# Performance work log

Hardware: AMD Instinct MI355X
Metric: run time of the kernel (lower is better)

The kernel has to match this reference:

```python
import jax, jax.numpy as jnp
import numpy as np

B, N, D_IN, D_OUT, R = 8, 1024, 256, 256, 4


def setup_inputs() -> dict:
    key = jax.random.key(0)
    ks = jax.random.split(key, 8)
    scale_in = 1.0 / np.sqrt(D_IN)
    scale_out = 1.0 / np.sqrt(2 * D_OUT)
    scale_g = 1.0 / np.sqrt(D_OUT)
    return {
        "node_features": jax.random.normal(ks[0], (B, N, D_IN), dtype=jnp.float32),
        "adj_matrix": jax.random.randint(ks[1], (B, R, N, N), 0, 2, dtype=jnp.int32),
        "rel_w": jax.random.uniform(ks[2], (R, D_OUT, D_IN), jnp.float32, -scale_in, scale_in),
        "rel_b": jax.random.uniform(ks[3], (R, D_OUT), jnp.float32, -scale_in, scale_in),
        "attn_w": jax.random.uniform(ks[4], (2 * D_OUT,), jnp.float32, -scale_out, scale_out),
        "attn_b": jax.random.uniform(ks[5], (), jnp.float32, -scale_out, scale_out),
        "gate_w": jax.random.uniform(ks[6], (D_OUT,), jnp.float32, -scale_g, scale_g),
        "gate_b": jax.random.uniform(ks[7], (), jnp.float32, -scale_g, scale_g),
    }


def reference(node_features, adj_matrix, rel_w, rel_b, attn_w, attn_b, gate_w, gate_b):
    # Per-relation projections: [B, R, N, D]
    feats = jnp.einsum('bni,rdi->brnd', node_features, rel_w) + rel_b[None, :, None, :]
    # attn_proj(cat([h_i, h_j])) == h_i @ w_i + h_j @ w_j + b  (linear over concat)
    d = feats.shape[-1]
    si = jnp.einsum('brnd,d->brn', feats, attn_w[:d])   # contribution of row node i
    sj = jnp.einsum('brnd,d->brn', feats, attn_w[d:])   # contribution of col node j
    score = si[:, :, :, None] + sj[:, :, None, :] + attn_b  # [B, R, N, N]
    score = jnp.where(adj_matrix == 0, jnp.float32(-1e9), score)
    attn = jax.nn.softmax(score, axis=-1)
    # Aggregate over relations: sum_r attn_r @ feats_r -> [B, N, D]
    agg = jnp.einsum('brnm,brmd->bnd', attn, feats)
    gate = jax.nn.sigmoid(jnp.einsum('bnd,d->bn', agg, gate_w) + gate_b)
    return gate[:, :, None] * agg
```

## Files before the change

### kernel.cpp

```cpp
#include <hip/hip_runtime.h>
#include <hip/hip_bf16.h>

#define B_ 8
#define N_ 1024
#define DIN 256
#define DOUT 256
#define R_ 4

typedef __attribute__((ext_vector_type(8))) short bf16x8;
typedef __attribute__((ext_vector_type(4))) float f32x4;
typedef __attribute__((ext_vector_type(4))) int i32x4;

__device__ __forceinline__ unsigned short f2bf(float f) {
    union { float f; unsigned int u; } v; v.f = f;
    unsigned int u = v.u;
    u += 0x7fffu + ((u >> 16) & 1u);
    return (unsigned short)(u >> 16);
}
__device__ __forceinline__ float bf2f(unsigned short h) {
    union { float f; unsigned int u; } v; v.u = ((unsigned int)h) << 16;
    return v.f;
}

__device__ __forceinline__ void gl_lds16(const void* g, void* l) {
    __builtin_amdgcn_global_load_lds(
        (const __attribute__((address_space(1))) unsigned int*)g,
        (__attribute__((address_space(3))) unsigned int*)l, 16, 0, 0);
}

__global__ __launch_bounds__(256) void k0_swz(const float* __restrict__ rw,
                                              unsigned short* __restrict__ swzW) {
    int t = blockIdx.x * 256 + threadIdx.x;
    int lane = t & 63, nb = (t >> 6) & 15, ks = (t >> 10) & 7, r = t >> 13;
    int m = lane & 15, q = lane >> 4;
    const float* src = rw + ((r * DOUT + nb * 16 + m) * DIN) + ks * 32 + q * 8;
    float4 v0 = *(const float4*)src;
    float4 v1 = *(const float4*)(src + 4);
    bf16x8 o;
    o[0] = (short)f2bf(v0.x); o[1] = (short)f2bf(v0.y);
    o[2] = (short)f2bf(v0.z); o[3] = (short)f2bf(v0.w);
    o[4] = (short)f2bf(v1.x); o[5] = (short)f2bf(v1.y);
    o[6] = (short)f2bf(v1.z); o[7] = (short)f2bf(v1.w);
    *(bf16x8*)(swzW + (long)t * 8) = o;
}

__global__ __launch_bounds__(256) void k1_proj(const float* __restrict__ node,
        const unsigned short* __restrict__ swzW, const float* __restrict__ rel_b,
        const float* __restrict__ attn_w,
        unsigned short* __restrict__ fswz, unsigned short* __restrict__ ebf) {
    __shared__ unsigned short Wbuf[2][8192];
    int bid = blockIdx.x;
    int nt = bid & 15, r = (bid >> 4) & 3, b = bid >> 6;
    int w = threadIdx.x >> 6, lane = threadIdx.x & 63;
    int m = lane & 15, q = lane >> 4;
    int n0 = nt * 64 + w * 16;

    const float* Abase = node + ((b * N_ + n0 + m) * DIN) + q * 8;
    const unsigned short* Wsrc = swzW + r * 65536;

#pragma unroll
    for (int i = 0; i < 4; i++)
        gl_lds16(Wsrc + (w * 4 + i) * 512 + lane * 8, &Wbuf[0][(w * 4 + i) * 512]);

    f32x4 acc[16];
#pragma unroll
    for (int i = 0; i < 16; i++) acc[i] = (f32x4)0.0f;

    float4 a0 = *(const float4*)(Abase);
    float4 a1 = *(const float4*)(Abase + 4);

    for (int ks = 0; ks < 8; ks++) {
        int cur = ks & 1;
        __syncthreads();
        if (ks < 7) {
#pragma unroll
            for (int i = 0; i < 4; i++)
                gl_lds16(Wsrc + ((ks + 1) * 16 + w * 4 + i) * 512 + lane * 8,
                         &Wbuf[cur ^ 1][(w * 4 + i) * 512]);
        }
        bf16x8 af;
        af[0] = (short)f2bf(a0.x); af[1] = (short)f2bf(a0.y);
        af[2] = (short)f2bf(a0.z); af[3] = (short)f2bf(a0.w);
        af[4] = (short)f2bf(a1.x); af[5] = (short)f2bf(a1.y);
        af[6] = (short)f2bf(a1.z); af[7] = (short)f2bf(a1.w);
        if (ks < 7) {
            a0 = *(const float4*)(Abase + (ks + 1) * 32);
            a1 = *(const float4*)(Abase + (ks + 1) * 32 + 4);
        }
#pragma unroll
        for (int nb = 0; nb < 16; nb++) {
            bf16x8 wf = *(const bf16x8*)(&Wbuf[cur][nb * 512 + lane * 8]);
            acc[nb] = __builtin_amdgcn_mfma_f32_16x16x32_bf16(af, wf, acc[nb], 0, 0, 0);
        }
    }

    float sj0 = 0.f, sj1 = 0.f, sj2 = 0.f, sj3 = 0.f;
    float bias[16], aw[16];
#pragma unroll
    for (int nb = 0; nb < 16; nb++) {
        int d = nb * 16 + m;
        bias[nb] = rel_b[r * DOUT + d];
        aw[nb] = attn_w[DOUT + d];
        sj0 += (acc[nb][0] + bias[nb]) * aw[nb];
        sj1 += (acc[nb][1] + bias[nb]) * aw[nb];
        sj2 += (acc[nb][2] + bias[nb]) * aw[nb];
        sj3 += (acc[nb][3] + bias[nb]) * aw[nb];
    }
#pragma unroll
    for (int mk = 1; mk <= 8; mk <<= 1) {
        sj0 += __shfl_xor(sj0, mk, 64);
        sj1 += __shfl_xor(sj1, mk, 64);
        sj2 += __shfl_xor(sj2, mk, 64);
        sj3 += __shfl_xor(sj3, mk, 64);
    }
    float e0 = __expf(sj0), e1 = __expf(sj1), e2 = __expf(sj2), e3 = __expf(sj3);

    int slice = b * R_ + r;
    int js = n0 >> 5;
    int jhi = (n0 >> 4) & 1;
    int qp = jhi * 2 + (q >> 1);
    int jj0 = (q & 1) * 4;
    unsigned short* fb = fswz + ((long)(slice * 32 + js) * 16) * 512
                       + qp * 128 + m * 8 + jj0;
#pragma unroll
    for (int nb = 0; nb < 16; nb++) {
        ushort4 o;
        o.x = f2bf((acc[nb][0] + bias[nb]) * e0);
        o.y = f2bf((acc[nb][1] + bias[nb]) * e1);
        o.z = f2bf((acc[nb][2] + bias[nb]) * e2);
        o.w = f2bf((acc[nb][3] + bias[nb]) * e3);
        *(ushort4*)(fb + nb * 512) = o;
    }
    if (m == 0) {
        ushort4 o;
        o.x = f2bf(e0); o.y = f2bf(e1); o.z = f2bf(e2); o.w = f2bf(e3);
        *(ushort4*)(ebf + slice * N_ + n0 + q * 4) = o;
    }
}

__global__ __launch_bounds__(256, 4) void k3_attn(const int* __restrict__ adj,
        const unsigned short* __restrict__ fswz, const unsigned short* __restrict__ ebf,
        unsigned short* __restrict__ aggU, float* __restrict__ lbuf) {
    __shared__ unsigned short Gbuf[2][8192];
    __shared__ unsigned short Ebuf[512];

    int bid = blockIdx.x;
    int slice = (bid & 7) * 4 + ((bid >> 3) & 3);
    int rest = bid >> 5;
    int it = rest & 15, jh = rest >> 4;
    int t = threadIdx.x, lane = t & 63, w = t >> 6;
    int m = lane & 15, q = lane >> 4;
    int i0b = it * 64;

    const unsigned short* fsl = fswz + ((size_t)(slice * 32 + jh * 16)) * 8192;
    const int* adjbase = adj + (size_t)slice * (N_ * N_)
                       + (size_t)(i0b + w * 16 + m) * N_ + jh * 512 + q * 8;
    const unsigned short* esl = ebf + slice * N_ + jh * 512;

#pragma unroll
    for (int i = 0; i < 4; i++)
        gl_lds16(fsl + (w * 4 + i) * 512 + lane * 8, &Gbuf[0][(w * 4 + i) * 512]);
    if (w == 0)
        gl_lds16(esl + lane * 8, &Ebuf[0]);

    i32x4 A0c = *(const i32x4*)(adjbase);
    i32x4 A1c = *(const i32x4*)(adjbase + 4);

    f32x4 acc[16];
#pragma unroll
    for (int i = 0; i < 16; i++) acc[i] = (f32x4)0.0f;
    float l = 0.f;

    for (int s = 0; s < 16; s++) {
        int cur = s & 1;
        __syncthreads();
        i32x4 A0n, A1n;
        if (s < 15) {
#pragma unroll
            for (int i = 0; i < 4; i++)
                gl_lds16(fsl + (size_t)(s + 1) * 8192 + (w * 4 + i) * 512 + lane * 8,
                         &Gbuf[cur ^ 1][(w * 4 + i) * 512]);
            A0n = *(const i32x4*)(adjbase + (s + 1) * 32);
            A1n = *(const i32x4*)(adjbase + (s + 1) * 32 + 4);
        }
        bf16x8 ev = *(const bf16x8*)(&Ebuf[s * 32 + q * 8]);
        int av[8] = {A0c.x, A0c.y, A0c.z, A0c.w, A1c.x, A1c.y, A1c.z, A1c.w};
        const int* ei = (const int*)&ev;
        bf16x8 af;
        int* afi = (int*)&af;
#pragma unroll
        for (int p = 0; p < 4; p++) {
            unsigned int msk = (av[2 * p] ? 0xffffu : 0u)
                             | (av[2 * p + 1] ? 0xffff0000u : 0u);
            afi[p] = (int)(msk & 0x3F803F80u);
            int me = ei[p] & (int)msk;
            union { int i; float f; } lo, hi;
            lo.i = me << 16;
            hi.i = me & (int)0xffff0000u;
            l += lo.f + hi.f;
        }
        const unsigned short* Gb = &Gbuf[cur][lane * 8];
#pragma unroll
        for (int nb = 0; nb < 16; nb++) {
            bf16x8 bfq = *(const bf16x8*)(Gb + nb * 512);
            acc[nb] = __builtin_amdgcn_mfma_f32_16x16x32_bf16(af, bfq, acc[nb], 0, 0, 0);
        }
        A0c = A0n; A1c = A1n;
    }

    l += __shfl_xor(l, 16, 64);
    l += __shfl_xor(l, 32, 64);
    int half = slice * 2 + jh;
    if (lane < 16)
        lbuf[half * N_ + i0b + w * 16 + lane] = l;

    unsigned short* ob = aggU + ((size_t)half * N_ + i0b + w * 16 + q * 4) * DOUT + m;
#pragma unroll
    for (int nb = 0; nb < 16; nb++) {
#pragma unroll
        for (int reg = 0; reg < 4; reg++)
            ob[(size_t)reg * DOUT + nb * 16] = f2bf(acc[nb][reg]);
    }
}

__global__ __launch_bounds__(256) void k4_out(const unsigned short* __restrict__ aggU,
        const float* __restrict__ lbuf, const float* __restrict__ gate_w,
        const float* __restrict__ gate_b, float* __restrict__ out) {
    __shared__ float red[4];
    int bid = blockIdx.x;
    int n = bid & 1023, b = bid >> 10;
    int d = threadIdx.x;
    float s = 0.f;
#pragma unroll
    for (int r = 0; r < R_; r++) {
        int sl = b * R_ + r;
        float a0 = bf2f(aggU[((size_t)(sl * 2 + 0) * N_ + n) * DOUT + d]);
        float a1 = bf2f(aggU[((size_t)(sl * 2 + 1) * N_ + n) * DOUT + d]);
        float lt = lbuf[(sl * 2 + 0) * N_ + n] + lbuf[(sl * 2 + 1) * N_ + n];
        float inv = (lt > 0.f) ? 1.0f / lt : 0.f;
        s += (a0 + a1) * inv;
    }
    float v = s * gate_w[d];
#pragma unroll
    for (int off = 32; off; off >>= 1) v += __shfl_down(v, off, 64);
    int lane = d & 63, wave = d >> 6;
    if (lane == 0) red[wave] = v;
    __syncthreads();
    float tot = red[0] + red[1] + red[2] + red[3];
    float g = 1.f / (1.f + __expf(-(tot + gate_b[0])));
    out[((long)(b * N_ + n)) * DOUT + d] = g * s;
}

extern "C" void kernel_launch(void* const* d_in, const int* in_sizes, int n_in,
                              void* d_out, int out_size, void* d_ws, size_t ws_size,
                              hipStream_t stream) {
    const float* node   = (const float*)d_in[0];
    const int*   adj    = (const int*)d_in[1];
    const float* rel_w  = (const float*)d_in[2];
    const float* rel_b  = (const float*)d_in[3];
    const float* attn_w = (const float*)d_in[4];
    const float* gate_w = (const float*)d_in[6];
    const float* gate_b = (const float*)d_in[7];
    float* out = (float*)d_out;

    char* ws = (char*)d_ws;
    unsigned short* swzW = (unsigned short*)ws;
    unsigned short* fswz = (unsigned short*)(ws + 524288);
    unsigned short* ebf  = (unsigned short*)(ws + 17301504);
    unsigned short* aggU = (unsigned short*)(ws + 17367040);
    float*          lbuf = (float*)(ws + 50921472);

    k0_swz<<<128, 256, 0, stream>>>(rel_w, swzW);
    k1_proj<<<512, 256, 0, stream>>>(node, swzW, rel_b, attn_w, fswz, ebf);
    k3_attn<<<1024, 256, 0, stream>>>(adj, fswz, ebf, aggU, lbuf);
    k4_out<<<8192, 256, 0, stream>>>(aggU, lbuf, gate_w, gate_b, out);
}
```

Measured before the change: 253.6 us.

## Split attention K-loop across wave pairs and normalize in-kernel, dropping half-partials

The attention kernel no longer splits the column range across blocks. Each block now covers 32 rows over all 1024 columns, and the two wave pairs take alternate 32-column steps. The pairs reduce their partial accumulators and row sums through LDS, and softmax normalization happens before the bf16 store. This halves the aggregate intermediate buffer, removes the lbuf array, and simplifies the output kernel's reads. The cost is that each wave idles on alternate steps and the loop has twice as many block-wide barriers.

```diff
diff --git a/kernel.cpp b/kernel.cpp
--- a/kernel.cpp
+++ b/kernel.cpp
@@ -140,106 +140,124 @@
 
 __global__ __launch_bounds__(256, 4) void k3_attn(const int* __restrict__ adj,
         const unsigned short* __restrict__ fswz, const unsigned short* __restrict__ ebf,
-        unsigned short* __restrict__ aggU, float* __restrict__ lbuf) {
+        unsigned short* __restrict__ aggN) {
     __shared__ unsigned short Gbuf[2][8192];
-    __shared__ unsigned short Ebuf[512];
+    __shared__ unsigned short Ebuf[1024];
+    __shared__ float Lx[2][64];
 
     int bid = blockIdx.x;
     int slice = (bid & 7) * 4 + ((bid >> 3) & 3);
-    int rest = bid >> 5;
-    int it = rest & 15, jh = rest >> 4;
+    int it = bid >> 5;
     int t = threadIdx.x, lane = t & 63, w = t >> 6;
     int m = lane & 15, q = lane >> 4;
-    int i0b = it * 64;
-
-    const unsigned short* fsl = fswz + ((size_t)(slice * 32 + jh * 16)) * 8192;
+    int g = w & 1;
+    int ph = w >> 1;
+    int i0 = it * 32 + g * 16;
+
+    const unsigned short* fsl = fswz + (size_t)slice * (32 * 8192);
     const int* adjbase = adj + (size_t)slice * (N_ * N_)
-                       + (size_t)(i0b + w * 16 + m) * N_ + jh * 512 + q * 8;
-    const unsigned short* esl = ebf + slice * N_ + jh * 512;
+                       + (size_t)(i0 + m) * N_ + q * 8;
+    const unsigned short* esl = ebf + slice * N_;
 
 #pragma unroll
     for (int i = 0; i < 4; i++)
         gl_lds16(fsl + (w * 4 + i) * 512 + lane * 8, &Gbuf[0][(w * 4 + i) * 512]);
-    if (w == 0)
-        gl_lds16(esl + lane * 8, &Ebuf[0]);
-
-    i32x4 A0c = *(const i32x4*)(adjbase);
-    i32x4 A1c = *(const i32x4*)(adjbase + 4);
+    if (w < 2)
+        gl_lds16(esl + w * 512 + lane * 8, &Ebuf[w * 512]);
+
+    i32x4 A0c = *(const i32x4*)(adjbase + ph * 32);
+    i32x4 A1c = *(const i32x4*)(adjbase + ph * 32 + 4);
 
     f32x4 acc[16];
 #pragma unroll
     for (int i = 0; i < 16; i++) acc[i] = (f32x4)0.0f;
     float l = 0.f;
 
-    for (int s = 0; s < 16; s++) {
+    for (int s = 0; s < 32; s++) {
         int cur = s & 1;
         __syncthreads();
-        i32x4 A0n, A1n;
-        if (s < 15) {
+        if (s < 31) {
 #pragma unroll
             for (int i = 0; i < 4; i++)
                 gl_lds16(fsl + (size_t)(s + 1) * 8192 + (w * 4 + i) * 512 + lane * 8,
                          &Gbuf[cur ^ 1][(w * 4 + i) * 512]);
-            A0n = *(const i32x4*)(adjbase + (s + 1) * 32);
-            A1n = *(const i32x4*)(adjbase + (s + 1) * 32 + 4);
-        }
-        bf16x8 ev = *(const bf16x8*)(&Ebuf[s * 32 + q * 8]);
-        int av[8] = {A0c.x, A0c.y, A0c.z, A0c.w, A1c.x, A1c.y, A1c.z, A1c.w};
-        const int* ei = (const int*)&ev;
-        bf16x8 af;
-        int* afi = (int*)&af;
-#pragma unroll
-        for (int p = 0; p < 4; p++) {
-            unsigned int msk = (av[2 * p] ? 0xffffu : 0u)
-                             | (av[2 * p + 1] ? 0xffff0000u : 0u);
-            afi[p] = (int)(msk & 0x3F803F80u);
-            int me = ei[p] & (int)msk;
-            union { int i; float f; } lo, hi;
-            lo.i = me << 16;
-            hi.i = me & (int)0xffff0000u;
-            l += lo.f + hi.f;
-        }
-        const unsigned short* Gb = &Gbuf[cur][lane * 8];
+        }
+        if ((s & 1) == ph) {
+            i32x4 A0n, A1n;
+            if (s < 30) {
+                A0n = *(const i32x4*)(adjbase + (s + 2) * 32);
+                A1n = *(const i32x4*)(adjbase + (s + 2) * 32 + 4);
+            }
+            bf16x8 ev = *(const bf16x8*)(&Ebuf[s * 32 + q * 8]);
+            int av[8] = {A0c.x, A0c.y, A0c.z, A0c.w, A1c.x, A1c.y, A1c.z, A1c.w};
+            const int* ei = (const int*)&ev;
+            bf16x8 af;
+            int* afi = (int*)&af;
+#pragma unroll
+            for (int p = 0; p < 4; p++) {
+                unsigned int msk = (av[2 * p] ? 0xffffu : 0u)
+                                 | (av[2 * p + 1] ? 0xffff0000u : 0u);
+                afi[p] = (int)(msk & 0x3F803F80u);
+                int me = ei[p] & (int)msk;
+                union { int i; float f; } lo, hi;
+                lo.i = me << 16;
+                hi.i = me & (int)0xffff0000u;
+                l += lo.f + hi.f;
+            }
+            const unsigned short* Gb = &Gbuf[cur][lane * 8];
+#pragma unroll
+            for (int nb = 0; nb < 16; nb++) {
+                bf16x8 bfq = *(const bf16x8*)(Gb + nb * 512);
+                acc[nb] = __builtin_amdgcn_mfma_f32_16x16x32_bf16(af, bfq, acc[nb], 0, 0, 0);
+            }
+            if (s < 30) { A0c = A0n; A1c = A1n; }
+        }
+    }
+
+    __syncthreads();
+    if (w >= 2) {
+        float* GF = (float*)&Gbuf[0][0];
+#pragma unroll
+        for (int nb = 0; nb < 16; nb++)
+            *(f32x4*)(&GF[g * 4096 + nb * 256 + lane * 4]) = acc[nb];
+        Lx[g][lane] = l;
+    }
+    __syncthreads();
+    if (w < 2) {
+        const float* GF = (const float*)&Gbuf[0][0];
+#pragma unroll
+        for (int nb = 0; nb < 16; nb++)
+            acc[nb] += *(const f32x4*)(&GF[g * 4096 + nb * 256 + lane * 4]);
+        l += Lx[g][lane];
+        l += __shfl_xor(l, 16, 64);
+        l += __shfl_xor(l, 32, 64);
+        float linv[4];
+#pragma unroll
+        for (int reg = 0; reg < 4; reg++) {
+            float lr = __shfl(l, q * 4 + reg, 64);
+            linv[reg] = (lr > 0.f) ? 1.0f / lr : 0.f;
+        }
+        unsigned short* ob = aggN + ((size_t)(slice * N_ + i0 + q * 4)) * DOUT + m;
 #pragma unroll
         for (int nb = 0; nb < 16; nb++) {
-            bf16x8 bfq = *(const bf16x8*)(Gb + nb * 512);
-            acc[nb] = __builtin_amdgcn_mfma_f32_16x16x32_bf16(af, bfq, acc[nb], 0, 0, 0);
-        }
-        A0c = A0n; A1c = A1n;
-    }
-
-    l += __shfl_xor(l, 16, 64);
-    l += __shfl_xor(l, 32, 64);
-    int half = slice * 2 + jh;
-    if (lane < 16)
-        lbuf[half * N_ + i0b + w * 16 + lane] = l;
-
-    unsigned short* ob = aggU + ((size_t)half * N_ + i0b + w * 16 + q * 4) * DOUT + m;
-#pragma unroll
-    for (int nb = 0; nb < 16; nb++) {
-#pragma unroll
-        for (int reg = 0; reg < 4; reg++)
-            ob[(size_t)reg * DOUT + nb * 16] = f2bf(acc[nb][reg]);
-    }
-}
-
-__global__ __launch_bounds__(256) void k4_out(const unsigned short* __restrict__ aggU,
-        const float* __restrict__ lbuf, const float* __restrict__ gate_w,
-        const float* __restrict__ gate_b, float* __restrict__ out) {
+#pragma unroll
+            for (int reg = 0; reg < 4; reg++)
+                ob[(size_t)reg * DOUT + nb * 16] = f2bf(acc[nb][reg] * linv[reg]);
+        }
+    }
+}
+
+__global__ __launch_bounds__(256) void k4_out(const unsigned short* __restrict__ aggN,
+        const float* __restrict__ gate_w, const float* __restrict__ gate_b,
+        float* __restrict__ out) {
     __shared__ float red[4];
     int bid = blockIdx.x;
     int n = bid & 1023, b = bid >> 10;
     int d = threadIdx.x;
     float s = 0.f;
 #pragma unroll
-    for (int r = 0; r < R_; r++) {
-        int sl = b * R_ + r;
-        float a0 = bf2f(aggU[((size_t)(sl * 2 + 0) * N_ + n) * DOUT + d]);
-        float a1 = bf2f(aggU[((size_t)(sl * 2 + 1) * N_ + n) * DOUT + d]);
-        float lt = lbuf[(sl * 2 + 0) * N_ + n] + lbuf[(sl * 2 + 1) * N_ + n];
-        float inv = (lt > 0.f) ? 1.0f / lt : 0.f;
-        s += (a0 + a1) * inv;
-    }
+    for (int r = 0; r < R_; r++)
+        s += bf2f(aggN[((size_t)((b * R_ + r) * N_ + n)) * DOUT + d]);
     float v = s * gate_w[d];
 #pragma unroll
     for (int off = 32; off; off >>= 1) v += __shfl_down(v, off, 64);
@@ -248,7 +266,7 @@
     __syncthreads();
     float tot = red[0] + red[1] + red[2] + red[3];
     float g = 1.f / (1.f + __expf(-(tot + gate_b[0])));
-    out[((long)(b * N_ + n)) * DOUT + d] = g * s;
+    out[((size_t)(b * N_ + n)) * DOUT + d] = g * s;
 }
 
 extern "C" void kernel_launch(void* const* d_in, const int* in_sizes, int n_in,
@@ -267,11 +285,10 @@
     unsigned short* swzW = (unsigned short*)ws;
     unsigned short* fswz = (unsigned short*)(ws + 524288);
     unsigned short* ebf  = (unsigned short*)(ws + 17301504);
-    unsigned short* aggU = (unsigned short*)(ws + 17367040);
-    float*          lbuf = (float*)(ws + 50921472);
+    unsigned short* aggN = (unsigned short*)(ws + 17367040);
 
     k0_swz<<<128, 256, 0, stream>>>(rel_w, swzW);
     k1_proj<<<512, 256, 0, stream>>>(node, swzW, rel_b, attn_w, fswz, ebf);
-    k3_attn<<<1024, 256, 0, stream>>>(adj, fswz, ebf, aggU, lbuf);
-    k4_out<<<8192, 256, 0, stream>>>(aggU, lbuf, gate_w, gate_b, out);
-}
+    k3_attn<<<1024, 256, 0, stream>>>(adj, fswz, ebf, aggN);
+    k4_out<<<8192, 256, 0, stream>>>(aggN, gate_w, gate_b, out);
+}
```

New measurement: 257.1 us. Within noise of the previous version (+1.4%).
